# Kernel tuning notes

Measured on AMD Instinct MI355X. Metric: run time of the kernel, lower is better.

## Reference

```python
import jax, jax.numpy as jnp
import numpy as np

SR = 24000
N_FFT = 1024
HOP = 320
N_MELS = 128
N_CB = 4
VOCAB = 1024
D_MODEL = 512


def _mel_fbanks():
    # torchaudio melscale_fbanks defaults: htk mel scale, norm=None, f_min=0, f_max=sr/2
    n_freqs = N_FFT // 2 + 1
    all_freqs = np.linspace(0.0, SR / 2.0, n_freqs)
    hz2mel = lambda f: 2595.0 * np.log10(1.0 + f / 700.0)
    m_pts = np.linspace(hz2mel(0.0), hz2mel(SR / 2.0), N_MELS + 2)
    f_pts = 700.0 * (10.0 ** (m_pts / 2595.0) - 1.0)
    f_diff = np.diff(f_pts)
    slopes = f_pts[None, :] - all_freqs[:, None]          # (n_freqs, n_mels+2)
    down = -slopes[:, :-2] / f_diff[:-1]
    up = slopes[:, 2:] / f_diff[1:]
    return np.maximum(0.0, np.minimum(down, up)).astype(np.float32)  # (n_freqs, n_mels)

_FB = jnp.asarray(_mel_fbanks())
# periodic Hann window (torch.hann_window default)
_WIN = jnp.asarray((0.5 * (1.0 - np.cos(2.0 * np.pi * np.arange(N_FFT) / N_FFT))).astype(np.float32))


def _log_mel(wav):
    # wav: (B, L). center=True STFT with reflect padding, power=2 spectrogram.
    pad = N_FFT // 2
    x = jnp.pad(wav, ((0, 0), (pad, pad)), mode='reflect')
    n_frames = 1 + (x.shape[1] - N_FFT) // HOP
    idx = HOP * jnp.arange(n_frames)[:, None] + jnp.arange(N_FFT)[None, :]
    frames = x[:, idx] * _WIN                              # (B, T, n_fft)
    spec = jnp.abs(jnp.fft.rfft(frames, axis=-1)) ** 2     # (B, T, n_freqs)
    mel = spec @ _FB                                       # (B, T, n_mels)
    return jnp.log(jnp.clip(mel, 1e-5))


def _conv1d(x, w, b):
    # x: (B, C, T), w: (O, I, 3), padding=1
    y = jax.lax.conv_general_dilated(x, w, window_strides=(1,), padding=((1, 1),),
                                     dimension_numbers=('NCH', 'OIH', 'NCH'))
    return y + b[None, :, None]


def setup_inputs() -> dict:
    key = jax.random.key(0)
    k = jax.random.split(key, 4)
    waveform = jax.random.normal(k[0], (16, 240000), dtype=jnp.float32)
    w1 = jax.random.normal(k[1], (256, N_MELS, 3), dtype=jnp.float32) * 0.05
    b1 = jnp.zeros((256,), dtype=jnp.float32)
    w2 = jax.random.normal(k[2], (D_MODEL, 256, 3), dtype=jnp.float32) * 0.05
    b2 = jnp.zeros((D_MODEL,), dtype=jnp.float32)
    codebooks = jax.random.normal(k[3], (N_CB, VOCAB, D_MODEL // N_CB), dtype=jnp.float32)
    return {"waveform": waveform, "w1": w1, "b1": b1, "w2": w2, "b2": b2, "codebooks": codebooks}


def reference(waveform, w1, b1, w2, b2, codebooks):
    logmel = _log_mel(waveform)                            # (B, T, n_mels)
    x = logmel.transpose(0, 2, 1)                          # (B, n_mels, T)
    h = jax.nn.gelu(_conv1d(x, w1, b1), approximate=False)
    feats = _conv1d(h, w2, b2).transpose(0, 2, 1)          # (B, T, D_MODEL)
    B, T, D = feats.shape
    f4 = feats.reshape(B, T, N_CB, D // N_CB)              # per-codebook slices
    x2 = jnp.sum(f4 * f4, axis=-1)[..., None]              # (B, T, K, 1)
    c2 = jnp.sum(codebooks * codebooks, axis=-1)           # (K, V)
    xc = jnp.einsum('btkd,kvd->btkv', f4, codebooks)       # (B, T, K, V)
    d2 = x2 - 2.0 * xc + c2[None, None]
    tokens = jnp.argmin(d2, axis=-1)                       # (B, T, K)
    return tokens.transpose(0, 2, 1).astype(jnp.int32)     # (B, n_codebooks, T)
```

## Files before the change

### kernel.cpp

```cpp
#include <hip/hip_runtime.h>
#include <hip/hip_bf16.h>
#include <float.h>

#define PI_D 3.14159265358979323846

#define LWAV 240000
#define TFR  751
#define BATCH 16
#define MROWS (BATCH * TFR)
#define NMEL 128
#define TFRP 753
#define PITCH2 12160
#define MTILES 95
#define MAXW 40

#define BSWZ(c) ((c) ^ ((((c) >> 5) & 3) << 2))

#define OFF_WIN    0u
#define OFF_TW512  4096u
#define OFF_UTW    8192u
#define OFF_C2MX   12304u
#define OFF_CNT    12352u
#define OFF_MELW   16384u
#define OFF_MELSL  36864u
#define OFF_WB1    40960u
#define OFF_WBH2   434176u
#define OFF_WBL2   1220608u
#define OFF_PB     434176u
#define OFF_C2     2007040u
#define OFF_CBH    2023424u
#define OFF_CBL    3072000u
#define OFF_X2     4120576u
#define OFF_HT     4317184u
#define OFF_FET    16777216u
#define OFF_LMT    OFF_FET
#define OFF_LIST   OFF_FET
#define OFF_WT2F   (OFF_FET + 262144u)
#define OFF_CBTF   18612224u
#define WS_NEEDED  41685000u

typedef unsigned short u16;
typedef __attribute__((ext_vector_type(8))) __bf16 bf16x8;
typedef __attribute__((ext_vector_type(4))) float f32x4;
union UB { uint4 u; bf16x8 v; };
union UA { u16 s[8]; bf16x8 v; };

__device__ __forceinline__ u16 bf16rne(float x) {
  unsigned u = __float_as_uint(x);
  return (u16)((u + 0x7FFFu + ((u >> 16) & 1u)) >> 16);
}
__device__ __forceinline__ float bf16tof(u16 h) {
  return __uint_as_float(((unsigned)h) << 16);
}

__device__ __forceinline__ int jobmap(int bid, int GP) {
  return (bid & 7) * GP + (bid >> 3);
}

__global__ void k_setup_tab(float* __restrict__ win, float2* __restrict__ tw512,
                            float2* __restrict__ utw) {
  int t = threadIdx.x;
  if (t < 1024) {
    double v = 0.5 * (1.0 - cos(2.0 * PI_D * (double)t / 1024.0));
    win[t] = (float)v;
  }
  if (t < 512) {
    double a = -2.0 * PI_D * (double)t / 512.0;
    tw512[t] = make_float2((float)cos(a), (float)sin(a));
  }
  if (t < 513) {
    double a = -2.0 * PI_D * (double)t / 1024.0;
    utw[t] = make_float2((float)cos(a), (float)sin(a));
  }
}

__device__ __forceinline__ double fpt_d(int j) {
  double melmax = 2595.0 * log10(1.0 + 12000.0 / 700.0);
  double mp = melmax * (double)j / 129.0;
  return 700.0 * (pow(10.0, mp / 2595.0) - 1.0);
}

__global__ void k_melw(float* __restrict__ melw, int2* __restrict__ melsl) {
  int m = threadIdx.x;
  double f0 = fpt_d(m), f1 = fpt_d(m + 1), f2 = fpt_d(m + 2);
  const double binw = 12000.0 / 512.0;
  int s = (int)floor(f0 / binw) + 1;
  if (s < 0) s = 0;
  int e = (int)ceil(f2 / binw) - 1;
  if (e > 512) e = 512;
  int len = e - s + 1;
  if (len < 0) len = 0;
  if (len > MAXW) len = MAXW;
  melsl[m] = make_int2(s, len);
  for (int j = 0; j < MAXW; ++j) {
    double freq = binw * (double)(s + j);
    double down = (freq - f0) / (f1 - f0);
    double up = (f2 - freq) / (f2 - f1);
    double v = fmin(down, up);
    v = fmax(0.0, v);
    melw[m * MAXW + j] = (j < len) ? (float)v : 0.f;
  }
}

__global__ void k_wt(const float* __restrict__ w, float* __restrict__ wt,
                     int O, int C) {
  int idx = blockIdx.x * 256 + threadIdx.x;
  int total = O * C * 3;
  if (idx >= total) return;
  int o = idx % O;
  int rest = idx / O;
  int i = rest % C;
  int dt = rest / C;
  wt[(dt * C + i) * O + o] = w[(o * C + i) * 3 + dt];
}

__global__ void k_wt2conv(const float* __restrict__ w2, u16* __restrict__ wbH2,
                          u16* __restrict__ wbL2) {
  int idx = blockIdx.x * 256 + threadIdx.x;
  if (idx >= 512 * 768) return;
  int o = idx / 768;
  int k = idx - o * 768;
  int dt = k >> 8, i = k & 255;
  float x = w2[(size_t)(o * 256 + i) * 3 + dt];
  u16 hh = bf16rne(x);
  wbH2[idx] = hh;
  wbL2[idx] = bf16rne(x - bf16tof(hh));
}

__global__ void k_wt2f(const float* __restrict__ w2, float* __restrict__ wt2f) {
  int idx = blockIdx.x * 256 + threadIdx.x;
  if (idx >= 768 * 512) return;
  int o = idx & 511, k = idx >> 9;
  int dt = k >> 8, i = k & 255;
  wt2f[idx] = w2[(size_t)(o * 256 + i) * 3 + dt];
}

__global__ void k_cbtf(const float* __restrict__ cbs, float* __restrict__ cbTf) {
  int idx = blockIdx.x * 256 + threadIdx.x;
  int v = idx & 1023;
  int d = (idx >> 10) & 127;
  int cb = idx >> 17;
  cbTf[idx] = cbs[(size_t)((cb << 10) + v) * 128 + d];
}

__global__ void k_c2(const float* __restrict__ cb, float* __restrict__ c2) {
  int v = blockIdx.x * 256 + threadIdx.x;
  if (v >= 4096) return;
  const float* r = cb + (size_t)v * 128;
  float s = 0.f;
#pragma unroll 8
  for (int i = 0; i < 128; ++i) s = fmaf(r[i], r[i], s);
  c2[v] = s;
}

__global__ void k_c2mx(const float* __restrict__ c2, float* __restrict__ c2mx,
                       unsigned* __restrict__ cnt) {
  __shared__ float red[256];
  int cb = blockIdx.x, tid = threadIdx.x;
  float m = 0.f;
  for (int v = tid; v < 1024; v += 256) m = fmaxf(m, c2[cb * 1024 + v]);
  red[tid] = m;
  __syncthreads();
  for (int s = 128; s > 0; s >>= 1) {
    if (tid < s) red[tid] = fmaxf(red[tid], red[tid + s]);
    __syncthreads();
  }
  if (tid == 0) {
    c2mx[cb] = red[0];
    if (cb == 0) *cnt = 0u;
  }
}

__global__ void k_cbconv(const float* __restrict__ cbs, u16* __restrict__ cbH,
                         u16* __restrict__ cbL) {
  int id = blockIdx.x * 256 + threadIdx.x;
  int v = id >> 5, d4 = (id & 31) * 4;
  float4 x = *(const float4*)(cbs + (size_t)v * 128 + d4);
  const float xs[4] = {x.x, x.y, x.z, x.w};
  unsigned wh[2], wl[2];
#pragma unroll
  for (int p = 0; p < 2; ++p) {
    u16 h0 = bf16rne(xs[2 * p]);
    u16 h1 = bf16rne(xs[2 * p + 1]);
    u16 l0 = bf16rne(xs[2 * p] - bf16tof(h0));
    u16 l1 = bf16rne(xs[2 * p + 1] - bf16tof(h1));
    wh[p] = (unsigned)h0 | ((unsigned)h1 << 16);
    wl[p] = (unsigned)l0 | ((unsigned)l1 << 16);
  }
  *(uint2*)(cbH + (size_t)v * 128 + d4) = make_uint2(wh[0], wh[1]);
  *(uint2*)(cbL + (size_t)v * 128 + d4) = make_uint2(wl[0], wl[1]);
}

__global__ void k_zerocols(float* __restrict__ a, int rows) {
  int tid = blockIdx.x * 256 + threadIdx.x;
  int col_id = tid & 31;
  int r = tid >> 5;
  if (r >= rows) return;
  int bq = col_id >> 1;
  int c = bq * TFRP + ((col_id & 1) ? 752 : 0);
  a[(size_t)r * PITCH2 + c] = 0.f;
}

__device__ __forceinline__ float2 cadd(float2 a, float2 b) { return make_float2(a.x + b.x, a.y + b.y); }
__device__ __forceinline__ float2 csub(float2 a, float2 b) { return make_float2(a.x - b.x, a.y - b.y); }
__device__ __forceinline__ float2 cmul(float2 a, float2 b) {
  return make_float2(a.x * b.x - a.y * b.y, a.x * b.y + a.y * b.x);
}
__device__ __forceinline__ float2 mulnegi(float2 a) { return make_float2(a.y, -a.x); }

__device__ __forceinline__ void dft8(const float2* d, float2* o) {
  const float S = 0.70710678118654752440f;
  float2 f0 = cadd(d[0], d[4]), f1 = csub(d[0], d[4]);
  float2 f2 = cadd(d[2], d[6]), f3 = csub(d[2], d[6]);
  float2 h0 = cadd(d[1], d[5]), h1 = csub(d[1], d[5]);
  float2 h2 = cadd(d[3], d[7]), h3 = csub(d[3], d[7]);
  float2 E0 = cadd(f0, f2), E2 = csub(f0, f2);
  float2 nif3 = mulnegi(f3);
  float2 E1 = cadd(f1, nif3), E3 = csub(f1, nif3);
  float2 O0 = cadd(h0, h2), O2 = csub(h0, h2);
  float2 nih3 = mulnegi(h3);
  float2 O1 = cadd(h1, nih3), O3 = csub(h1, nih3);
  float2 w1o = make_float2(S * (O1.x + O1.y), S * (O1.y - O1.x));
  float2 w2o = mulnegi(O2);
  float2 w3o = make_float2(S * (O3.y - O3.x), -S * (O3.x + O3.y));
  o[0] = cadd(E0, O0);  o[4] = csub(E0, O0);
  o[1] = cadd(E1, w1o); o[5] = csub(E1, w1o);
  o[2] = cadd(E2, w2o); o[6] = csub(E2, w2o);
  o[3] = cadd(E3, w3o); o[7] = csub(E3, w3o);
}

__device__ __forceinline__ float powspec(const float2* Z, const float2* __restrict__ utw,
                                         int k) {
  float2 Zk = Z[k & 511];
  float2 Zm = Z[(512 - k) & 511];
  float2 ut = utw[k];
  float fer = 0.5f * (Zk.x + Zm.x);
  float fei = 0.5f * (Zk.y - Zm.y);
  float fo_r = 0.5f * (Zk.y + Zm.y);
  float fo_i = -0.5f * (Zk.x - Zm.x);
  float xr = fer + ut.x * fo_r - ut.y * fo_i;
  float xi = fei + ut.x * fo_i + ut.y * fo_r;
  return xr * xr + xi * xi;
}

__global__ __launch_bounds__(256) void k_logmel3(
    const float* __restrict__ wav, const float* __restrict__ win,
    const float2* __restrict__ tw512, const float2* __restrict__ utw,
    const float* __restrict__ melw, const int2* __restrict__ melsl,
    float* __restrict__ lmT) {
  __shared__ float2 zbuf[4][512];
  __shared__ float pbuf[4][516];
  __shared__ float mex[128][5];

  const int w = threadIdx.x >> 6;
  const int t = threadIdx.x & 63;
  const int bq = blockIdx.x / 188;
  const int t0 = (blockIdx.x % 188) * 4;
  const int tt = min(t0 + w, TFR - 1);
  const float* wv = wav + (size_t)bq * LWAV;
  float2* Z = zbuf[w];
  float* p = pbuf[w];

  const int base = tt * 320 - 512;

  float2 c[8];
  if (base >= 0 && base + 1024 <= LWAV) {
    const float2* wv2 = (const float2*)(wv + base);
    const float2* wn2 = (const float2*)win;
#pragma unroll
    for (int j = 0; j < 8; ++j) {
      int mm = t + 64 * j;
      float2 xv = wv2[mm];
      float2 wn = wn2[mm];
      c[j] = make_float2(xv.x * wn.x, xv.y * wn.y);
    }
  } else {
#pragma unroll
    for (int j = 0; j < 8; ++j) {
      int mm = t + 64 * j;
      int n0 = base + 2 * mm, n1 = n0 + 1;
      int j0 = n0 < 0 ? -n0 : (n0 >= LWAV ? 2 * LWAV - 2 - n0 : n0);
      int j1 = n1 < 0 ? -n1 : (n1 >= LWAV ? 2 * LWAV - 2 - n1 : n1);
      c[j] = make_float2(wv[j0] * win[2 * mm], wv[j1] * win[2 * mm + 1]);
    }
  }

  float2 e[8];
  dft8(c, e);
#pragma unroll
  for (int pp = 1; pp < 8; ++pp) e[pp] = cmul(e[pp], tw512[(t * pp) & 511]);
#pragma unroll
  for (int pp = 0; pp < 8; ++pp) Z[pp * 64 + (t ^ (pp << 3))] = e[pp];
  asm volatile("s_waitcnt lgkmcnt(0)" ::: "memory");

  const int P = t >> 3, M = t & 7;
  float2 g[8];
#pragma unroll
  for (int v = 0; v < 8; ++v) g[v] = Z[P * 64 + ((M + 8 * v) ^ (P << 3))];
  asm volatile("s_waitcnt lgkmcnt(0)" ::: "memory");

  float2 y[8];
  dft8(g, y);
#pragma unroll
  for (int aa = 1; aa < 8; ++aa) y[aa] = cmul(y[aa], tw512[(8 * M * aa) & 511]);
#pragma unroll
  for (int aa = 0; aa < 8; ++aa) Z[aa * 64 + (((M << 3) + P) ^ (aa << 3))] = y[aa];
  asm volatile("s_waitcnt lgkmcnt(0)" ::: "memory");

  float2 yv[8];
#pragma unroll
  for (int u = 0; u < 8; ++u) yv[u] = Z[P * 64 + (((u << 3) + M) ^ (P << 3))];
  asm volatile("s_waitcnt lgkmcnt(0)" ::: "memory");

  float2 X[8];
  dft8(yv, X);
#pragma unroll
  for (int bb = 0; bb < 8; ++bb) Z[bb * 64 + t] = X[bb];
  asm volatile("s_waitcnt lgkmcnt(0)" ::: "memory");

#pragma unroll
  for (int j = 0; j < 8; ++j) {
    int k = t + 64 * j;
    p[k] = powspec(Z, utw, k);
  }
  if (t == 0) p[512] = powspec(Z, utw, 512);
  asm volatile("s_waitcnt lgkmcnt(0)" ::: "memory");

#pragma unroll
  for (int h = 0; h < 2; ++h) {
    int m = 2 * t + h;
    int2 sl = melsl[m];
    float acc = 0.f;
    const float* wrow = melw + m * MAXW;
    for (int j = 0; j < sl.y; ++j) acc = fmaf(p[sl.x + j], wrow[j], acc);
    mex[m][w] = logf(fmaxf(acc, 1e-5f));
  }
  __syncthreads();
  if (threadIdx.x < 128) {
    int cc = threadIdx.x;
    float* op = lmT + (size_t)cc * PITCH2 + (size_t)bq * TFRP + 1 + t0;
    op[0] = mex[cc][0];
    op[1] = mex[cc][1];
    op[2] = mex[cc][2];
    op[3] = mex[cc][3];
  }
}

template <int C, int N, int BN, bool GELU>
__global__ __launch_bounds__(256) void k_conv64(const float* __restrict__ in,
                                                const float* __restrict__ wt,
                                                const float* __restrict__ bias,
                                                float* __restrict__ out) {
  constexpr int K = 3 * C;
  constexpr int NC = BN / 16;
  __shared__ float At[32 * 64];
  __shared__ float Bt[32 * BN];
  const int j = jobmap(blockIdx.x, 95);
  const int m0 = (j >> 2) * 64;
  const int n0 = (j & 3) * BN;
  const int tid = threadIdx.x;
  const int tm = tid >> 4, tn = tid & 15;

  int bco[NC / 4];
#pragma unroll
  for (int i = 0; i < NC / 4; ++i) bco[i] = BSWZ(tn * NC + i * 4);

  float acc[4][NC] = {};

  for (int k0 = 0; k0 < K; k0 += 32) {
    const int dt = k0 / C;
    const int i0 = k0 - dt * C;
    const float* asrc = in + (size_t)i0 * PITCH2 + (m0 + dt - 1);
    const float* bsrc = wt + (size_t)k0 * N + n0;
#pragma unroll
    for (int h = 0; h < 2; ++h) {
      const int id = tid + h * 256;
      const int r = id >> 4, cf = (id & 15) * 4;
      const float* ap = asrc + (size_t)r * PITCH2 + cf;
      *(float4*)&At[r * 64 + cf] = make_float4(ap[0], ap[1], ap[2], ap[3]);
    }
#pragma unroll
    for (int h = 0; h < BN / 32; ++h) {
      const int id = tid + h * 256;
      const int r = id / (BN / 4), cf = (id % (BN / 4)) * 4;
      *(float4*)&Bt[r * BN + BSWZ(cf)] = *(const float4*)(bsrc + (size_t)r * N + cf);
    }
    __syncthreads();
#pragma unroll
    for (int kc = 0; kc < 32; ++kc) {
      float4 a = *(const float4*)&At[kc * 64 + tm * 4];
      float av[4] = {a.x, a.y, a.z, a.w};
      float bv[NC];
#pragma unroll
      for (int i = 0; i < NC / 4; ++i) {
        float4 b = *(const float4*)&Bt[kc * BN + bco[i]];
        bv[i * 4] = b.x; bv[i * 4 + 1] = b.y; bv[i * 4 + 2] = b.z; bv[i * 4 + 3] = b.w;
      }
#pragma unroll
      for (int r = 0; r < 4; ++r)
#pragma unroll
        for (int cq = 0; cq < NC; ++cq) acc[r][cq] = fmaf(av[r], bv[cq], acc[r][cq]);
    }
    __syncthreads();
  }

#pragma unroll
  for (int cq = 0; cq < NC; ++cq) {
    const int n = n0 + tn * NC + cq;
    const float bb = bias[n];
    float vv[4];
#pragma unroll
    for (int r = 0; r < 4; ++r) {
      float v = acc[r][cq] + bb;
      if (GELU) v = 0.5f * v * (1.0f + erff(v * 0.7071067811865476f));
      vv[r] = v;
    }
    *(float4*)(out + (size_t)n * PITCH2 + m0 + tm * 4) =
        make_float4(vv[0], vv[1], vv[2], vv[3]);
  }
}

#define MFMA16(a, b, c) __builtin_amdgcn_mfma_f32_16x16x32_bf16((a), (b), (c), 0, 0, 0)

#define C2M_ISSUE_A(dst, cc) do {                                           \
    const int kc0_ = (cc) * 32;                                             \
    const int dt_ = kc0_ >> 8, i0_ = kc0_ & 255;                            \
    const float* hb_ = hT + (size_t)(i0_ + g * 8) * PITCH2                  \
                       + m0 + mhalf * 32 + ln + dt_ - 1;                    \
    _Pragma("unroll") for (int mi_ = 0; mi_ < 2; ++mi_)                     \
      _Pragma("unroll") for (int j_ = 0; j_ < 8; ++j_)                      \
        dst[mi_][j_] = hb_[(size_t)j_ * PITCH2 + mi_ * 16];                 \
  } while (0)

#define C2M_ISSUE_B(cc) do {                                                \
    const int kc0_ = (cc) * 32;                                             \
    _Pragma("unroll") for (int h2_ = 0; h2_ < 2; ++h2_) {                   \
      const int id_ = tid + h2_ * 256;                                      \
      const int nn_ = id_ >> 2, part_ = id_ & 3;                            \
      const size_t src_ = (size_t)(n0 + nn_) * 768 + kc0_ + part_ * 8;      \
      rBh[h2_] = *(const uint4*)(wbH2 + src_);                              \
      rBl[h2_] = *(const uint4*)(wbL2 + src_);                              \
    }                                                                       \
  } while (0)

#define C2M_COMMIT_B(buf) do {                                              \
    _Pragma("unroll") for (int h2_ = 0; h2_ < 2; ++h2_) {                   \
      const int id_ = tid + h2_ * 256;                                      \
      const int nn_ = id_ >> 2, part_ = id_ & 3;                            \
      *(uint4*)&bHs[buf][nn_ * 40 + part_ * 8] = rBh[h2_];                  \
      *(uint4*)&bLs[buf][nn_ * 40 + part_ * 8] = rBl[h2_];                  \
    }                                                                       \
  } while (0)

__global__ __launch_bounds__(256) void k_conv2m(
    const float* __restrict__ hT,
    const u16* __restrict__ wbH2, const u16* __restrict__ wbL2,
    const float* __restrict__ b2, float* __restrict__ feT) {
  __shared__ __align__(16) u16 bHs[2][128 * 40];
  __shared__ __align__(16) u16 bLs[2][128 * 40];
  const int j = jobmap(blockIdx.x, 95);
  const int mt = j >> 2;
  const int nq = j & 3;
  const int tid = threadIdx.x;
  const int w = tid >> 6, l = tid & 63;
  const int mhalf = w & 1, nhalf = w >> 1;
  const int g = l >> 4, ln = l & 15;
  const int m0 = mt * 64;
  const int n0 = nq * 128;

  f32x4 acc[2][4];
#pragma unroll
  for (int mi = 0; mi < 2; ++mi)
#pragma unroll
    for (int vi = 0; vi < 4; ++vi) acc[mi][vi] = (f32x4){0.f, 0.f, 0.f, 0.f};

  float rA[2][8], rA2[2][8];
  uint4 rBh[2], rBl[2];

  C2M_ISSUE_A(rA, 0);
  C2M_ISSUE_B(0);
  C2M_COMMIT_B(0);
  __syncthreads();

  int cur = 0;
  for (int cc = 0; cc < 24; ++cc) {
    const bool more = (cc + 1 < 24);
    if (more) { C2M_ISSUE_B(cc + 1); C2M_ISSUE_A(rA2, cc + 1); }
    UA aH[2], aL[2];
#pragma unroll
    for (int mi = 0; mi < 2; ++mi)
#pragma unroll
      for (int jx = 0; jx < 8; ++jx) {
        u16 hh = bf16rne(rA[mi][jx]);
        aH[mi].s[jx] = hh;
        aL[mi].s[jx] = bf16rne(rA[mi][jx] - bf16tof(hh));
      }
    const u16* bH = bHs[cur];
    const u16* bL = bLs[cur];
#pragma unroll
    for (int vi = 0; vi < 4; ++vi) {
      const int nn = nhalf * 64 + vi * 16 + ln;
      UB bh, bl;
      bh.u = *(const uint4*)&bH[nn * 40 + g * 8];
      bl.u = *(const uint4*)&bL[nn * 40 + g * 8];
#pragma unroll
      for (int mi = 0; mi < 2; ++mi) {
        acc[mi][vi] = MFMA16(aH[mi].v, bh.v, acc[mi][vi]);
        acc[mi][vi] = MFMA16(aH[mi].v, bl.v, acc[mi][vi]);
        acc[mi][vi] = MFMA16(aL[mi].v, bh.v, acc[mi][vi]);
      }
    }
    if (more) {
      C2M_COMMIT_B(cur ^ 1);
      __syncthreads();
      cur ^= 1;
#pragma unroll
      for (int mi = 0; mi < 2; ++mi)
#pragma unroll
        for (int jx = 0; jx < 8; ++jx) rA[mi][jx] = rA2[mi][jx];
    }
  }

#pragma unroll
  for (int vi = 0; vi < 4; ++vi) {
    const int nn = n0 + nhalf * 64 + vi * 16 + ln;
    const float bb = b2[nn];
#pragma unroll
    for (int mi = 0; mi < 2; ++mi) {
      f32x4 A = acc[mi][vi];
      *(float4*)(feT + (size_t)nn * PITCH2 + m0 + mhalf * 32 + mi * 16 + g * 4) =
          make_float4(A[0] + bb, A[1] + bb, A[2] + bb, A[3] + bb);
    }
  }
}

__global__ void k_x2(const float* __restrict__ feT, float* __restrict__ x2) {
  int m = blockIdx.x * 256 + threadIdx.x;
  int cb = blockIdx.y;
  if (m >= PITCH2) return;
  const float* p = feT + (size_t)(cb * 128) * PITCH2 + m;
  float s = 0.f;
#pragma unroll 4
  for (int r = 0; r < 128; ++r) {
    float a = p[(size_t)r * PITCH2];
    s = fmaf(a, a, s);
  }
  x2[(size_t)cb * PITCH2 + m] = s;
}

__global__ __launch_bounds__(256) void k_vqmfma(
    const float* __restrict__ feT,
    const u16* __restrict__ cbH, const u16* __restrict__ cbL,
    const float* __restrict__ c2, float4* __restrict__ pb) {
  __shared__ __align__(16) u16 bHs[64 * 128];
  __shared__ __align__(16) u16 bLs[64 * 128];
  __shared__ float trip[64][2][4];

  const int j = jobmap(blockIdx.x, 190);
  const int mt = j >> 3;
  const int cb = (j & 7) >> 1;
  const int vh = j & 1;
  const int tid = threadIdx.x;
  const int w = tid >> 6, l = tid & 63;
  const int mhalf = w & 1, vhalf = w >> 1;
  const int m0 = mt * 64;
  const int q0 = vh * 8, q1 = q0 + 8;

  UA aH[2][4], aL[2][4];
  {
    const int g = l >> 4;
    const float* fb = feT + (size_t)(cb * 128 + (g << 3)) * PITCH2
                      + m0 + mhalf * 32 + (l & 15);
#pragma unroll
    for (int mi = 0; mi < 2; ++mi) {
#pragma unroll
      for (int ks = 0; ks < 4; ++ks) {
#pragma unroll
        for (int jx = 0; jx < 8; ++jx) {
          float x = fb[(size_t)(ks * 32 + jx) * PITCH2 + mi * 16];
          u16 hh = bf16rne(x);
          aH[mi][ks].s[jx] = hh;
          aL[mi][ks].s[jx] = bf16rne(x - bf16tof(hh));
        }
      }
    }
  }

  {
    const u16* gh = cbH + (size_t)(cb * 1024 + q0 * 64) * 128;
    const u16* gl = cbL + (size_t)(cb * 1024 + q0 * 64) * 128;
#pragma unroll
    for (int h = 0; h < 4; ++h) {
      int id = tid + h * 256;
      int row = id >> 4, c16 = id & 15;
      int go = row * 128 + c16 * 8;
      int so = row * 128 + ((c16 * 8) ^ ((row & 7) << 3));
      *(uint4*)&bHs[so] = *(const uint4*)&gh[go];
      *(uint4*)&bLs[so] = *(const uint4*)&gl[go];
    }
  }
  __syncthreads();

  float sb1[8], sb2[8];
  int si1[8];
#pragma unroll
  for (int st = 0; st < 8; ++st) { sb1[st] = FLT_MAX; sb2[st] = FLT_MAX; si1[st] = 0; }

  f32x4 acc[2][2];
#pragma unroll
  for (int mi = 0; mi < 2; ++mi)
#pragma unroll
    for (int vi = 0; vi < 2; ++vi) acc[mi][vi] = (f32x4){0.f, 0.f, 0.f, 0.f};

  const float* c2b = c2 + cb * 1024;

  for (int q = q0; q < q1; ++q) {
#pragma unroll
    for (int ks = 0; ks < 4; ++ks) {
      const int kbx = (ks * 32 + ((l >> 4) << 3)) ^ ((l & 7) << 3);
      const int rb = vhalf * 32 + (l & 15);
      UB b0h, b0l, b1h, b1l;
      b0h.u = *(const uint4*)&bHs[rb * 128 + kbx];
      b0l.u = *(const uint4*)&bLs[rb * 128 + kbx];
      b1h.u = *(const uint4*)&bHs[(rb + 16) * 128 + kbx];
      b1l.u = *(const uint4*)&bLs[(rb + 16) * 128 + kbx];
      acc[0][0] = MFMA16(aH[0][ks].v, b0h.v, acc[0][0]);
      acc[0][0] = MFMA16(aH[0][ks].v, b0l.v, acc[0][0]);
      acc[0][0] = MFMA16(aL[0][ks].v, b0h.v, acc[0][0]);
      acc[0][1] = MFMA16(aH[0][ks].v, b1h.v, acc[0][1]);
      acc[0][1] = MFMA16(aH[0][ks].v, b1l.v, acc[0][1]);
      acc[0][1] = MFMA16(aL[0][ks].v, b1h.v, acc[0][1]);
      acc[1][0] = MFMA16(aH[1][ks].v, b0h.v, acc[1][0]);
      acc[1][0] = MFMA16(aH[1][ks].v, b0l.v, acc[1][0]);
      acc[1][0] = MFMA16(aL[1][ks].v, b0h.v, acc[1][0]);
      acc[1][1] = MFMA16(aH[1][ks].v, b1h.v, acc[1][1]);
      acc[1][1] = MFMA16(aH[1][ks].v, b1l.v, acc[1][1]);
      acc[1][1] = MFMA16(aL[1][ks].v, b1h.v, acc[1][1]);
    }

#pragma unroll
    for (int mi = 0; mi < 2; ++mi) {
#pragma unroll
      for (int vi = 0; vi < 2; ++vi) {
        const int vg = q * 64 + vhalf * 32 + vi * 16 + (l & 15);
        const float cv = c2b[vg];
        f32x4 A = acc[mi][vi];
#pragma unroll
        for (int jx = 0; jx < 4; ++jx) {
          const float s = fmaf(-2.f, A[jx], cv);
          const int st = mi * 4 + jx;
          if (s < sb1[st]) { sb2[st] = sb1[st]; sb1[st] = s; si1[st] = vg; }
          else { sb2[st] = fminf(sb2[st], s); }
        }
        acc[mi][vi] = (f32x4){0.f, 0.f, 0.f, 0.f};
      }
    }

    if (q + 1 < q1) {
      __syncthreads();
      const u16* gh = cbH + (size_t)(cb * 1024 + (q + 1) * 64) * 128;
      const u16* gl = cbL + (size_t)(cb * 1024 + (q + 1) * 64) * 128;
#pragma unroll
      for (int h = 0; h < 4; ++h) {
        int id = tid + h * 256;
        int row = id >> 4, c16 = id & 15;
        int go = row * 128 + c16 * 8;
        int so = row * 128 + ((c16 * 8) ^ ((row & 7) << 3));
        *(uint4*)&bHs[so] = *(const uint4*)&gh[go];
        *(uint4*)&bLs[so] = *(const uint4*)&gl[go];
      }
      __syncthreads();
    }
  }

#pragma unroll
  for (int st = 0; st < 8; ++st) {
    float B1 = sb1[st], B2 = sb2[st];
    int I1 = si1[st];
#pragma unroll
    for (int off = 1; off < 16; off <<= 1) {
      float oB1 = __shfl_xor(B1, off, 64);
      int oI1 = __shfl_xor(I1, off, 64);
      float oB2 = __shfl_xor(B2, off, 64);
      bool take = (oB1 < B1) || (oB1 == B1 && oI1 < I1);
      float lose = take ? B1 : oB1;
      B2 = fminf(fminf(B2, oB2), lose);
      if (take) { B1 = oB1; I1 = oI1; }
    }
    if ((l & 15) == 0) {
      int row = mhalf * 32 + (st >> 2) * 16 + (l >> 4) * 4 + (st & 3);
      trip[row][vhalf][0] = B1;
      trip[row][vhalf][1] = __int_as_float(I1);
      trip[row][vhalf][2] = B2;
    }
  }
  __syncthreads();
  if (tid < 64) {
    float B1 = trip[tid][0][0], B2 = trip[tid][0][2];
    int I1 = __float_as_int(trip[tid][0][1]);
    float oB1 = trip[tid][1][0], oB2 = trip[tid][1][2];
    int oI1 = __float_as_int(trip[tid][1][1]);
    bool take = (oB1 < B1) || (oB1 == B1 && oI1 < I1);
    float lose = take ? B1 : oB1;
    B2 = fminf(fminf(B2, oB2), lose);
    if (take) { B1 = oB1; I1 = oI1; }
    pb[(size_t)(cb * 2 + vh) * PITCH2 + m0 + tid] =
        make_float4(B1, __int_as_float(I1), B2, 0.f);
  }
}

#define LISTCAP 48064u
__global__ void k_vqsel(const float4* __restrict__ pb, const float* __restrict__ x2,
                        const float* __restrict__ c2mx, unsigned* __restrict__ cnt,
                        unsigned* __restrict__ list, int* __restrict__ out) {
  int ml = blockIdx.x * 256 + threadIdx.x;
  int cb = blockIdx.y;
  if (ml >= MROWS) return;
  int b = ml / TFR, t = ml - b * TFR;
  int mp = b * TFRP + 1 + t;

  float B1 = FLT_MAX, B2 = FLT_MAX;
  int I1 = 0;
#pragma unroll
  for (int vh = 0; vh < 2; ++vh) {
    float4 e = pb[(size_t)(cb * 2 + vh) * PITCH2 + mp];
    float a1 = e.x, a2 = e.z;
    int ai = __float_as_int(e.y);
    if (a1 < B1 || (a1 == B1 && ai < I1)) {
      B2 = fminf(B1, a2);
      B1 = a1;
      I1 = ai;
    } else {
      B2 = fminf(B2, a1);
    }
  }

  float xx = x2[(size_t)cb * PITCH2 + mp];
  float cm = c2mx[cb];
  float eps = 1.5e-4f * sqrtf(fmaxf(xx * cm, 0.f)) + 6e-5f * (xx + cm);
  if (!(B2 - B1 > eps)) {
    unsigned k = atomicAdd(cnt, 1u);
    if (k < LISTCAP) list[k] = ((unsigned)cb << 14) | (unsigned)mp;
  }
  out[((size_t)b * 4 + cb) * TFR + t] = I1;
}

__global__ __launch_bounds__(256) void k_vqfix(
    const unsigned* __restrict__ cnt, const unsigned* __restrict__ list,
    const float* __restrict__ hT, const float* __restrict__ wt2f,
    const float* __restrict__ b2, const float* __restrict__ cbTf,
    const float* __restrict__ c2, int* __restrict__ out) {
  __shared__ float hcol[768];
  __shared__ float xs[128];
  __shared__ float rd[256];
  __shared__ int ri[256];
  const int tid = threadIdx.x;
  const unsigned n = min(*cnt, LISTCAP);
  for (unsigned i = blockIdx.x; i < n; i += gridDim.x) {
    unsigned e = list[i];
    int cb = e >> 14;
    int mp = e & 0x3FFF;
    __syncthreads();
#pragma unroll
    for (int h = 0; h < 3; ++h) {
      int kk = tid + h * 256;
      int dt = kk >> 8, ii = kk & 255;
      hcol[kk] = hT[(size_t)ii * PITCH2 + (mp + dt - 1)];
    }
    __syncthreads();
    if (tid < 128) {
      int o = cb * 128 + tid;
      float dot = 0.f;
      for (int k = 0; k < 768; ++k)
        dot = fmaf(hcol[k], wt2f[(size_t)k * 512 + o], dot);
      xs[tid] = dot + b2[o];
    }
    __syncthreads();
    float xx = 0.f;
#pragma unroll 8
    for (int d = 0; d < 128; ++d) xx = fmaf(xs[d], xs[d], xx);
    float dot4[4] = {0.f, 0.f, 0.f, 0.f};
    const float* cbase = cbTf + (size_t)(cb * 128) * 1024 + tid;
    for (int d = 0; d < 128; ++d) {
      const float* cp = cbase + (size_t)d * 1024;
      float x = xs[d];
#pragma unroll
      for (int vv = 0; vv < 4; ++vv) dot4[vv] = fmaf(x, cp[vv * 256], dot4[vv]);
    }
    float bd = FLT_MAX;
    int bi = 0;
#pragma unroll
    for (int vv = 0; vv < 4; ++vv) {
      int v = vv * 256 + tid;
      float d2 = xx - 2.f * dot4[vv] + c2[cb * 1024 + v];
      if (d2 < bd) { bd = d2; bi = v; }
    }
    rd[tid] = bd;
    ri[tid] = bi;
    __syncthreads();
    for (int s = 128; s > 0; s >>= 1) {
      if (tid < s) {
        float od = rd[tid + s];
        int oi = ri[tid + s];
        if (od < rd[tid] || (od == rd[tid] && oi < ri[tid])) { rd[tid] = od; ri[tid] = oi; }
      }
      __syncthreads();
    }
    if (tid == 0) {
      int b = mp / TFRP, t = mp % TFRP - 1;
      out[((size_t)b * 4 + cb) * TFR + t] = ri[0];
    }
  }
}

extern "C" void kernel_launch(void* const* d_in, const int* in_sizes, int n_in,
                              void* d_out, int out_size, void* d_ws, size_t ws_size,
                              hipStream_t stream) {
  if (ws_size < WS_NEEDED) return;

  const float* wav = (const float*)d_in[0];
  const float* w1 = (const float*)d_in[1];
  const float* b1 = (const float*)d_in[2];
  const float* w2 = (const float*)d_in[3];
  const float* b2 = (const float*)d_in[4];
  const float* cbs = (const float*)d_in[5];
  int* out = (int*)d_out;

  char* W = (char*)d_ws;
  float* win = (float*)(W + OFF_WIN);
  float2* tw512 = (float2*)(W + OFF_TW512);
  float2* utw = (float2*)(W + OFF_UTW);
  float* c2mx = (float*)(W + OFF_C2MX);
  unsigned* cnt = (unsigned*)(W + OFF_CNT);
  float* melw = (float*)(W + OFF_MELW);
  int2* melsl = (int2*)(W + OFF_MELSL);
  float* wb1 = (float*)(W + OFF_WB1);
  u16* wbH2 = (u16*)(W + OFF_WBH2);
  u16* wbL2 = (u16*)(W + OFF_WBL2);
  float4* pb = (float4*)(W + OFF_PB);
  unsigned* list = (unsigned*)(W + OFF_LIST);
  float* wt2f = (float*)(W + OFF_WT2F);
  float* cbTf = (float*)(W + OFF_CBTF);
  float* c2 = (float*)(W + OFF_C2);
  u16* cbH = (u16*)(W + OFF_CBH);
  u16* cbL = (u16*)(W + OFF_CBL);
  float* x2 = (float*)(W + OFF_X2);
  float* hT = (float*)(W + OFF_HT);
  float* feT = (float*)(W + OFF_FET);
  float* lmT = (float*)(W + OFF_LMT);

  k_setup_tab<<<1, 1024, 0, stream>>>(win, tw512, utw);
  k_melw<<<1, 128, 0, stream>>>(melw, melsl);
  k_wt<<<(256 * 128 * 3 + 255) / 256, 256, 0, stream>>>(w1, wb1, 256, 128);
  k_wt2conv<<<1536, 256, 0, stream>>>(w2, wbH2, wbL2);
  k_c2<<<16, 256, 0, stream>>>(cbs, c2);
  k_c2mx<<<4, 256, 0, stream>>>(c2, c2mx, cnt);
  k_cbconv<<<512, 256, 0, stream>>>(cbs, cbH, cbL);

  k_logmel3<<<16 * 188, 256, 0, stream>>>(wav, win, tw512, utw, melw, melsl, lmT);
  k_zerocols<<<(128 * 32 + 255) / 256, 256, 0, stream>>>(lmT, 128);
  k_conv64<128, 256, 64, true><<<760, 256, 0, stream>>>(lmT, wb1, b1, hT);
  k_zerocols<<<(256 * 32 + 255) / 256, 256, 0, stream>>>(hT, 256);
  k_conv2m<<<760, 256, 0, stream>>>(hT, wbH2, wbL2, b2, feT);

  k_x2<<<dim3((PITCH2 + 255) / 256, 4), 256, 0, stream>>>(feT, x2);
  k_vqmfma<<<1520, 256, 0, stream>>>(feT, cbH, cbL, c2, pb);
  k_wt2f<<<1536, 256, 0, stream>>>(w2, wt2f);
  k_cbtf<<<2048, 256, 0, stream>>>(cbs, cbTf);
  k_vqsel<<<dim3((MROWS + 255) / 256, 4), 256, 0, stream>>>(pb, x2, c2mx, cnt, list, out);
  k_vqfix<<<2048, 256, 0, stream>>>(cnt, list, hT, wt2f, b2, cbTf, c2, out);
}
```

Baseline: 269.3 us.

## Double-buffer codebook tiles in VQ kernel and raise wave priority around MFMAs

The VQ distance kernel now double-buffers its codebook hi/lo tiles in shared memory. The next tile is prefetched into registers before the MFMA loop and written to the alternate buffer afterwards, so one barrier per iteration replaces two and global latency overlaps compute. s_setprio is raised around the MFMA sections of both the conv2 and VQ kernels. This doubles the VQ kernel's LDS use, to 64KB for the B tiles, and adds 32 VGPRs of staging, which may reduce occupancy.

```diff
diff --git a/kernel.cpp b/kernel.cpp
--- a/kernel.cpp
+++ b/kernel.cpp
@@ -497,6 +497,7 @@
       }
     const u16* bH = bHs[cur];
     const u16* bL = bLs[cur];
+    __builtin_amdgcn_s_setprio(1);
 #pragma unroll
     for (int vi = 0; vi < 4; ++vi) {
       const int nn = nhalf * 64 + vi * 16 + ln;
@@ -510,6 +511,7 @@
         acc[mi][vi] = MFMA16(aL[mi].v, bh.v, acc[mi][vi]);
       }
     }
+    __builtin_amdgcn_s_setprio(0);
     if (more) {
       C2M_COMMIT_B(cur ^ 1);
       __syncthreads();
@@ -548,12 +550,33 @@
   x2[(size_t)cb * PITCH2 + m] = s;
 }
 
+#define VQ_ISSUE_B(qq) do {                                                 \
+    const u16* gh_ = cbH + (size_t)(cb * 1024 + (qq) * 64) * 128;           \
+    const u16* gl_ = cbL + (size_t)(cb * 1024 + (qq) * 64) * 128;           \
+    _Pragma("unroll") for (int h_ = 0; h_ < 4; ++h_) {                      \
+      int id_ = tid + h_ * 256;                                             \
+      int go_ = (id_ >> 4) * 128 + (id_ & 15) * 8;                          \
+      rBh[h_] = *(const uint4*)&gh_[go_];                                   \
+      rBl[h_] = *(const uint4*)&gl_[go_];                                   \
+    }                                                                       \
+  } while (0)
+
+#define VQ_COMMIT_B(buf) do {                                               \
+    _Pragma("unroll") for (int h_ = 0; h_ < 4; ++h_) {                      \
+      int id_ = tid + h_ * 256;                                             \
+      int row_ = id_ >> 4, c16_ = id_ & 15;                                 \
+      int so_ = row_ * 128 + ((c16_ * 8) ^ ((row_ & 7) << 3));              \
+      *(uint4*)&bHs[buf][so_] = rBh[h_];                                    \
+      *(uint4*)&bLs[buf][so_] = rBl[h_];                                    \
+    }                                                                       \
+  } while (0)
+
 __global__ __launch_bounds__(256) void k_vqmfma(
     const float* __restrict__ feT,
     const u16* __restrict__ cbH, const u16* __restrict__ cbL,
     const float* __restrict__ c2, float4* __restrict__ pb) {
-  __shared__ __align__(16) u16 bHs[64 * 128];
-  __shared__ __align__(16) u16 bLs[64 * 128];
+  __shared__ __align__(16) u16 bHs[2][64 * 128];
+  __shared__ __align__(16) u16 bLs[2][64 * 128];
   __shared__ float trip[64][2][4];
 
   const int j = jobmap(blockIdx.x, 190);
@@ -586,19 +609,9 @@
     }
   }
 
-  {
-    const u16* gh = cbH + (size_t)(cb * 1024 + q0 * 64) * 128;
-    const u16* gl = cbL + (size_t)(cb * 1024 + q0 * 64) * 128;
-#pragma unroll
-    for (int h = 0; h < 4; ++h) {
-      int id = tid + h * 256;
-      int row = id >> 4, c16 = id & 15;
-      int go = row * 128 + c16 * 8;
-      int so = row * 128 + ((c16 * 8) ^ ((row & 7) << 3));
-      *(uint4*)&bHs[so] = *(const uint4*)&gh[go];
-      *(uint4*)&bLs[so] = *(const uint4*)&gl[go];
-    }
-  }
+  uint4 rBh[4], rBl[4];
+  VQ_ISSUE_B(q0);
+  VQ_COMMIT_B(0);
   __syncthreads();
 
   float sb1[8], sb2[8];
@@ -614,16 +627,22 @@
 
   const float* c2b = c2 + cb * 1024;
 
+  int cur = 0;
   for (int q = q0; q < q1; ++q) {
+    const bool more = (q + 1 < q1);
+    if (more) VQ_ISSUE_B(q + 1);
+    const u16* bH = bHs[cur];
+    const u16* bL = bLs[cur];
+    __builtin_amdgcn_s_setprio(1);
 #pragma unroll
     for (int ks = 0; ks < 4; ++ks) {
       const int kbx = (ks * 32 + ((l >> 4) << 3)) ^ ((l & 7) << 3);
       const int rb = vhalf * 32 + (l & 15);
       UB b0h, b0l, b1h, b1l;
-      b0h.u = *(const uint4*)&bHs[rb * 128 + kbx];
-      b0l.u = *(const uint4*)&bLs[rb * 128 + kbx];
-      b1h.u = *(const uint4*)&bHs[(rb + 16) * 128 + kbx];
-      b1l.u = *(const uint4*)&bLs[(rb + 16) * 128 + kbx];
+      b0h.u = *(const uint4*)&bH[rb * 128 + kbx];
+      b0l.u = *(const uint4*)&bL[rb * 128 + kbx];
+      b1h.u = *(const uint4*)&bH[(rb + 16) * 128 + kbx];
+      b1l.u = *(const uint4*)&bL[(rb + 16) * 128 + kbx];
       acc[0][0] = MFMA16(aH[0][ks].v, b0h.v, acc[0][0]);
       acc[0][0] = MFMA16(aH[0][ks].v, b0l.v, acc[0][0]);
       acc[0][0] = MFMA16(aL[0][ks].v, b0h.v, acc[0][0]);
@@ -637,6 +656,7 @@
       acc[1][1] = MFMA16(aH[1][ks].v, b1l.v, acc[1][1]);
       acc[1][1] = MFMA16(aL[1][ks].v, b1h.v, acc[1][1]);
     }
+    __builtin_amdgcn_s_setprio(0);
 
 #pragma unroll
     for (int mi = 0; mi < 2; ++mi) {
@@ -656,20 +676,10 @@
       }
     }
 
-    if (q + 1 < q1) {
+    if (more) {
+      VQ_COMMIT_B(cur ^ 1);
       __syncthreads();
-      const u16* gh = cbH + (size_t)(cb * 1024 + (q + 1) * 64) * 128;
-      const u16* gl = cbL + (size_t)(cb * 1024 + (q + 1) * 64) * 128;
-#pragma unroll
-      for (int h = 0; h < 4; ++h) {
-        int id = tid + h * 256;
-        int row = id >> 4, c16 = id & 15;
-        int go = row * 128 + c16 * 8;
-        int so = row * 128 + ((c16 * 8) ^ ((row & 7) << 3));
-        *(uint4*)&bHs[so] = *(const uint4*)&gh[go];
-        *(uint4*)&bLs[so] = *(const uint4*)&gl[go];
-      }
-      __syncthreads();
+      cur ^= 1;
     }
   }
 
```

Result: slower. 328.4 us (+21.9%).
